# Optimization experiments

Hardware: AMD Instinct MI355X
Metric: run time of the kernel (lower is better)

## Reference

```python
import jax, jax.numpy as jnp
import numpy as np

HIDDEN = 1024
NUM_CLASSES = 10
NUM_GAUSSIANS = 8
IN_FEATURES = 16
HEADS = NUM_CLASSES * NUM_GAUSSIANS * IN_FEATURES * 2  # 2560 tiny Linear(hidden,1) heads


def setup_inputs() -> dict:
    key = jax.random.key(0)
    kx, kw, kb = jax.random.split(key, 3)
    x = jax.random.normal(kx, (8192, HIDDEN), dtype=jnp.float32)
    # Stacked weights of the 2560 per-head Linear(hidden,1) layers.
    bound = 1.0 / np.sqrt(HIDDEN)
    W = jax.random.uniform(kw, (HIDDEN, HEADS), minval=-bound, maxval=bound, dtype=jnp.float32)
    b = jax.random.uniform(kb, (HEADS,), minval=-bound, maxval=bound, dtype=jnp.float32)
    return {"x": x, "W": W, "b": b}


def reference(x, W, b):
    batch = x.shape[0]
    # Fused form of the Python loop of Linear(hidden,1)+Sigmoid per head.
    z = jax.nn.sigmoid(x @ W + b)  # [batch, HEADS]
    return z.reshape(batch, NUM_CLASSES, NUM_GAUSSIANS, IN_FEATURES, 2)
```

## Files before the change

kernel.cpp:

```cpp
#include <hip/hip_runtime.h>
#include <hip/hip_bf16.h>

#define HIDDEN 1024
#define HEADS  2560

#define BM 128
#define BN 160
#define BK 64
#define NT (HIDDEN / BK)
#define ABYT (BM * BK * 2)
#define BBYT (BN * BK * 2)
#define BUFSZ (ABYT + BBYT)

typedef float  f32x4  __attribute__((ext_vector_type(4)));
typedef __bf16 bf16x8 __attribute__((ext_vector_type(8)));
typedef __bf16 bf16x4 __attribute__((ext_vector_type(4)));

__device__ __forceinline__ void gload_lds16(const void* g, void* l) {
    __builtin_amdgcn_global_load_lds(
        (const __attribute__((address_space(1))) unsigned int*)g,
        (__attribute__((address_space(3))) unsigned int*)l, 16, 0, 0);
}
__device__ __forceinline__ unsigned swz(unsigned x) {
    return x ^ (((x >> 7) & 7u) << 4);
}

__global__ __launch_bounds__(256)
void cvt_all(const float* __restrict__ x, const float* __restrict__ W,
             __bf16* __restrict__ xc, __bf16* __restrict__ Wt, int n8)
{
    if (blockIdx.x < 640) {
        __shared__ __bf16 tile[64][72];
        const int t  = threadIdx.x;
        const int n0 = (blockIdx.x % 40) * 64;
        const int k0 = (blockIdx.x / 40) * 64;

        #pragma unroll
        for (int i = 0; i < 4; ++i) {
            const int k    = (t >> 4) + i * 16;
            const int col4 = (t & 15) * 4;
            const float4 v = *reinterpret_cast<const float4*>(
                W + (size_t)(k0 + k) * HEADS + n0 + col4);
            bf16x4 h;
            h[0] = (__bf16)v.x; h[1] = (__bf16)v.y; h[2] = (__bf16)v.z; h[3] = (__bf16)v.w;
            *reinterpret_cast<bf16x4*>(&tile[k][col4]) = h;
        }
        __syncthreads();
        #pragma unroll
        for (int i = 0; i < 4; ++i) {
            const int n  = (t >> 4) + i * 16;
            const int k4 = (t & 15) * 4;
            bf16x4 h;
            h[0] = tile[k4 + 0][n]; h[1] = tile[k4 + 1][n];
            h[2] = tile[k4 + 2][n]; h[3] = tile[k4 + 3][n];
            *reinterpret_cast<bf16x4*>(Wt + (size_t)(n0 + n) * HIDDEN + k0 + k4) = h;
        }
    } else {
        int idx    = (blockIdx.x - 640) * blockDim.x + threadIdx.x;
        int stride = (gridDim.x - 640) * blockDim.x;
        for (int i = idx; i < n8; i += stride) {
            const float4 a = *reinterpret_cast<const float4*>(x + (size_t)i * 8);
            const float4 b = *reinterpret_cast<const float4*>(x + (size_t)i * 8 + 4);
            bf16x8 h;
            h[0] = (__bf16)a.x; h[1] = (__bf16)a.y; h[2] = (__bf16)a.z; h[3] = (__bf16)a.w;
            h[4] = (__bf16)b.x; h[5] = (__bf16)b.y; h[6] = (__bf16)b.z; h[7] = (__bf16)b.w;
            *reinterpret_cast<bf16x8*>(xc + (size_t)i * 8) = h;
        }
    }
}

__global__ __launch_bounds__(512, 4)
void gemm_dl2(const __bf16* __restrict__ A, const __bf16* __restrict__ Bt,
              const float* __restrict__ bias, float* __restrict__ out)
{
    __shared__ char lds[2 * BUFSZ];

    const int t    = threadIdx.x;
    const int lane = t & 63;
    const int w    = t >> 6;
    const int wr   = w & 3;
    const int wc   = w >> 2;
    const int lhi  = lane >> 4;
    const int llo  = lane & 15;

    const int bid = blockIdx.x;
    const int by  = (bid & 7) * 2 + ((bid >> 3) & 1);
    const int bx  = bid >> 4;
    const int bm0 = bx * BM;
    const int bn0 = by * BN;

    const unsigned d0 = (unsigned)(t * 16);
    const unsigned L0 = swz(d0);
    const char* asrc0 = (const char*)A  + (size_t)(bm0 + (L0 >> 7)) * (HIDDEN * 2) + (L0 & 127);
    const char* bsrc0 = (const char*)Bt + (size_t)(bn0 + (L0 >> 7)) * (HIDDEN * 2) + (L0 & 127);
    const unsigned dt = 16384u + (unsigned)(t * 16);
    const unsigned Lt = swz(dt);
    const char* bsrct = (const char*)Bt + (size_t)(bn0 + (Lt >> 7)) * (HIDDEN * 2) + (Lt & 127);

    char* adst0 = (char*)lds + d0;
    char* bdst0 = (char*)lds + ABYT + d0;
    char* bdstt = (char*)lds + ABYT + dt;

    const unsigned xa = (unsigned)((llo & 7) << 4);
    const unsigned klo[2] = { ((unsigned)(lhi * 16)) ^ xa,
                              ((unsigned)(64 + lhi * 16)) ^ xa };
    const unsigned rowA = (unsigned)((wr * 32 + llo) * 128);
    const unsigned rowB = (unsigned)ABYT + (unsigned)((wc * 80 + llo) * 128);

    f32x4 acc[2][5];
    #pragma unroll
    for (int m = 0; m < 2; ++m)
        #pragma unroll
        for (int n = 0; n < 5; ++n)
            acc[m][n] = f32x4{0.f, 0.f, 0.f, 0.f};

    gload_lds16(asrc0,          adst0);
    gload_lds16(asrc0 + 131072, adst0 + 8192);
    gload_lds16(bsrc0,          bdst0);
    gload_lds16(bsrc0 + 131072, bdst0 + 8192);
    if (w < 4) gload_lds16(bsrct, bdstt);
    asm volatile("s_waitcnt vmcnt(0)" ::: "memory");
    __builtin_amdgcn_s_barrier();

    for (int k = 0; k < NT; ++k) {
        const char* buf  = lds + (k & 1) * BUFSZ;
        const unsigned nb = (unsigned)(((k + 1) & 1) * BUFSZ);
        const int   koff = (k + 1) * 128;

        if (k + 1 < NT) {
            gload_lds16(asrc0 + koff,          adst0 + nb);
            gload_lds16(asrc0 + koff + 131072, adst0 + nb + 8192);
            gload_lds16(bsrc0 + koff,          bdst0 + nb);
            gload_lds16(bsrc0 + koff + 131072, bdst0 + nb + 8192);
            if (w < 4) gload_lds16(bsrct + koff, bdstt + nb);
        }

        #pragma unroll
        for (int kk = 0; kk < 2; ++kk) {
            bf16x8 af[2], bfr[5];
            #pragma unroll
            for (int m = 0; m < 2; ++m)
                af[m]  = *(const bf16x8*)(buf + rowA + m * 2048 + klo[kk]);
            #pragma unroll
            for (int n = 0; n < 5; ++n)
                bfr[n] = *(const bf16x8*)(buf + rowB + n * 2048 + klo[kk]);
            #pragma unroll
            for (int m = 0; m < 2; ++m)
                #pragma unroll
                for (int n = 0; n < 5; ++n)
                    acc[m][n] = __builtin_amdgcn_mfma_f32_16x16x32_bf16(
                        af[m], bfr[n], acc[m][n], 0, 0, 0);
        }

        asm volatile("s_waitcnt vmcnt(0)" ::: "memory");
        __builtin_amdgcn_s_barrier();
    }

    #pragma unroll
    for (int n = 0; n < 5; ++n) {
        const int col  = bn0 + wc * 80 + n * 16 + llo;
        const float bv = bias[col];
        #pragma unroll
        for (int m = 0; m < 2; ++m) {
            const int row0 = bm0 + wr * 32 + m * 16 + lhi * 4;
            #pragma unroll
            for (int r = 0; r < 4; ++r) {
                const float z = acc[m][n][r] + bv;
                out[(size_t)(row0 + r) * HEADS + col] = __fdividef(1.0f, 1.0f + __expf(-z));
            }
        }
    }
}

#define FBM 128
#define FBN 128
#define FBK 32
#define FLDK 40

__global__ __launch_bounds__(256)
void lch_gemm(const float* __restrict__ x, const float* __restrict__ W,
              const float* __restrict__ b, float* __restrict__ out)
{
    __shared__ __bf16 As[FBM][FLDK];
    __shared__ __bf16 Bs[FBN][FLDK];

    const int t   = threadIdx.x;
    const int bm0 = blockIdx.x * FBM;
    const int bn0 = blockIdx.y * FBN;
    const int lane = t & 63;
    const int wid  = t >> 6;
    const int wr   = wid >> 1;
    const int wc   = wid & 1;
    const int lhi  = lane >> 4;
    const int llo  = lane & 15;

    f32x4 acc[4][4];
    #pragma unroll
    for (int i = 0; i < 4; ++i)
        #pragma unroll
        for (int j = 0; j < 4; ++j)
            acc[i][j] = f32x4{0.f, 0.f, 0.f, 0.f};

    const int bn_col  = t & 127;
    const int bk_base = (t >> 7) * 16;

    for (int k0 = 0; k0 < HIDDEN; k0 += FBK) {
        #pragma unroll
        for (int i = 0; i < 4; ++i) {
            const int f   = t + i * 256;
            const int row = f >> 3;
            const int c4  = (f & 7) * 4;
            const float4 v = *reinterpret_cast<const float4*>(
                x + (size_t)(bm0 + row) * HIDDEN + k0 + c4);
            bf16x4 h;
            h[0] = (__bf16)v.x; h[1] = (__bf16)v.y;
            h[2] = (__bf16)v.z; h[3] = (__bf16)v.w;
            *reinterpret_cast<bf16x4*>(&As[row][c4]) = h;
        }
        {
            const float* wp = W + (size_t)(k0 + bk_base) * HEADS + bn0 + bn_col;
            bf16x8 h0, h1;
            #pragma unroll
            for (int i = 0; i < 8; ++i) h0[i] = (__bf16)wp[(size_t)i * HEADS];
            #pragma unroll
            for (int i = 0; i < 8; ++i) h1[i] = (__bf16)wp[(size_t)(i + 8) * HEADS];
            *reinterpret_cast<bf16x8*>(&Bs[bn_col][bk_base])     = h0;
            *reinterpret_cast<bf16x8*>(&Bs[bn_col][bk_base + 8]) = h1;
        }
        __syncthreads();

        bf16x8 af[4], bfr[4];
        #pragma unroll
        for (int i = 0; i < 4; ++i)
            af[i] = *reinterpret_cast<const bf16x8*>(&As[wr * 64 + i * 16 + llo][lhi * 8]);
        #pragma unroll
        for (int j = 0; j < 4; ++j)
            bfr[j] = *reinterpret_cast<const bf16x8*>(&Bs[wc * 64 + j * 16 + llo][lhi * 8]);
        #pragma unroll
        for (int i = 0; i < 4; ++i)
            #pragma unroll
            for (int j = 0; j < 4; ++j)
                acc[i][j] = __builtin_amdgcn_mfma_f32_16x16x32_bf16(
                    af[i], bfr[j], acc[i][j], 0, 0, 0);
        __syncthreads();
    }

    #pragma unroll
    for (int j = 0; j < 4; ++j) {
        const int col  = bn0 + wc * 64 + j * 16 + llo;
        const float bv = b[col];
        #pragma unroll
        for (int i = 0; i < 4; ++i) {
            const int row0 = bm0 + wr * 64 + i * 16 + lhi * 4;
            #pragma unroll
            for (int r = 0; r < 4; ++r) {
                const float z = acc[i][j][r] + bv;
                out[(size_t)(row0 + r) * HEADS + col] = 1.0f / (1.0f + __expf(-z));
            }
        }
    }
}

extern "C" void kernel_launch(void* const* d_in, const int* in_sizes, int n_in,
                              void* d_out, int out_size, void* d_ws, size_t ws_size,
                              hipStream_t stream) {
    const float* x = (const float*)d_in[0];
    const float* W = (const float*)d_in[1];
    const float* b = (const float*)d_in[2];
    float* out     = (float*)d_out;

    const int M = in_sizes[0] / HIDDEN;

    const size_t xc_bytes = (size_t)M * HIDDEN * sizeof(__bf16);
    const size_t wt_bytes = (size_t)HEADS * HIDDEN * sizeof(__bf16);

    if (ws_size >= xc_bytes + wt_bytes && (M % BM) == 0) {
        __bf16* xc = (__bf16*)d_ws;
        __bf16* Wt = (__bf16*)((char*)d_ws + xc_bytes);

        cvt_all<<<640 + 2048, 256, 0, stream>>>(x, W, xc, Wt, M * HIDDEN / 8);

        const int nwg = (M / BM) * (HEADS / BN);
        gemm_dl2<<<nwg, 512, 0, stream>>>(xc, Wt, b, out);
    } else {
        dim3 grid(M / FBM, HEADS / FBN);
        lch_gemm<<<grid, dim3(256), 0, stream>>>(x, W, b, out);
    }
}
```

Before: 66.83 us.

## Fuse x fp32-to-bf16 conversion into GEMM A-tile loads

The separate pre-pass that converts x to bf16 in workspace is removed. The GEMM now loads fp32 x directly into registers, converts it, and writes the bf16 tile into swizzled LDS, with the writes issued after the MFMA loop to overlap load latency. This avoids a full write and re-read of the bf16 copy of x. In exchange, each GEMM block re-reads fp32 x, which is twice the bytes, across 16 column blocks, and adds register pressure plus a register-staged path in place of the direct global-to-LDS load.

```diff
diff --git a/kernel.cpp b/kernel.cpp
--- a/kernel.cpp
+++ b/kernel.cpp
@@ -24,54 +24,46 @@
 __device__ __forceinline__ unsigned swz(unsigned x) {
     return x ^ (((x >> 7) & 7u) << 4);
 }
+__device__ __forceinline__ bf16x8 cvt8(float4 a, float4 b) {
+    bf16x8 h;
+    h[0] = (__bf16)a.x; h[1] = (__bf16)a.y; h[2] = (__bf16)a.z; h[3] = (__bf16)a.w;
+    h[4] = (__bf16)b.x; h[5] = (__bf16)b.y; h[6] = (__bf16)b.z; h[7] = (__bf16)b.w;
+    return h;
+}
 
 __global__ __launch_bounds__(256)
-void cvt_all(const float* __restrict__ x, const float* __restrict__ W,
-             __bf16* __restrict__ xc, __bf16* __restrict__ Wt, int n8)
+void cvt_w(const float* __restrict__ W, __bf16* __restrict__ Wt)
 {
-    if (blockIdx.x < 640) {
-        __shared__ __bf16 tile[64][72];
-        const int t  = threadIdx.x;
-        const int n0 = (blockIdx.x % 40) * 64;
-        const int k0 = (blockIdx.x / 40) * 64;
-
-        #pragma unroll
-        for (int i = 0; i < 4; ++i) {
-            const int k    = (t >> 4) + i * 16;
-            const int col4 = (t & 15) * 4;
-            const float4 v = *reinterpret_cast<const float4*>(
-                W + (size_t)(k0 + k) * HEADS + n0 + col4);
-            bf16x4 h;
-            h[0] = (__bf16)v.x; h[1] = (__bf16)v.y; h[2] = (__bf16)v.z; h[3] = (__bf16)v.w;
-            *reinterpret_cast<bf16x4*>(&tile[k][col4]) = h;
-        }
-        __syncthreads();
-        #pragma unroll
-        for (int i = 0; i < 4; ++i) {
-            const int n  = (t >> 4) + i * 16;
-            const int k4 = (t & 15) * 4;
-            bf16x4 h;
-            h[0] = tile[k4 + 0][n]; h[1] = tile[k4 + 1][n];
-            h[2] = tile[k4 + 2][n]; h[3] = tile[k4 + 3][n];
-            *reinterpret_cast<bf16x4*>(Wt + (size_t)(n0 + n) * HIDDEN + k0 + k4) = h;
-        }
-    } else {
-        int idx    = (blockIdx.x - 640) * blockDim.x + threadIdx.x;
-        int stride = (gridDim.x - 640) * blockDim.x;
-        for (int i = idx; i < n8; i += stride) {
-            const float4 a = *reinterpret_cast<const float4*>(x + (size_t)i * 8);
-            const float4 b = *reinterpret_cast<const float4*>(x + (size_t)i * 8 + 4);
-            bf16x8 h;
-            h[0] = (__bf16)a.x; h[1] = (__bf16)a.y; h[2] = (__bf16)a.z; h[3] = (__bf16)a.w;
-            h[4] = (__bf16)b.x; h[5] = (__bf16)b.y; h[6] = (__bf16)b.z; h[7] = (__bf16)b.w;
-            *reinterpret_cast<bf16x8*>(xc + (size_t)i * 8) = h;
-        }
+    __shared__ __bf16 tile[64][72];
+    const int t  = threadIdx.x;
+    const int n0 = (blockIdx.x % 40) * 64;
+    const int k0 = (blockIdx.x / 40) * 64;
+
+    #pragma unroll
+    for (int i = 0; i < 4; ++i) {
+        const int k    = (t >> 4) + i * 16;
+        const int col4 = (t & 15) * 4;
+        const float4 v = *reinterpret_cast<const float4*>(
+            W + (size_t)(k0 + k) * HEADS + n0 + col4);
+        bf16x4 h;
+        h[0] = (__bf16)v.x; h[1] = (__bf16)v.y; h[2] = (__bf16)v.z; h[3] = (__bf16)v.w;
+        *reinterpret_cast<bf16x4*>(&tile[k][col4]) = h;
+    }
+    __syncthreads();
+    #pragma unroll
+    for (int i = 0; i < 4; ++i) {
+        const int n  = (t >> 4) + i * 16;
+        const int k4 = (t & 15) * 4;
+        bf16x4 h;
+        h[0] = tile[k4 + 0][n]; h[1] = tile[k4 + 1][n];
+        h[2] = tile[k4 + 2][n]; h[3] = tile[k4 + 3][n];
+        *reinterpret_cast<bf16x4*>(Wt + (size_t)(n0 + n) * HIDDEN + k0 + k4) = h;
     }
 }
 
 __global__ __launch_bounds__(512, 4)
-void gemm_dl2(const __bf16* __restrict__ A, const __bf16* __restrict__ Bt,
-              const float* __restrict__ bias, float* __restrict__ out)
+void gemm_fx(const float* __restrict__ x, const __bf16* __restrict__ Bt,
+             const float* __restrict__ bias, float* __restrict__ out)
 {
     __shared__ char lds[2 * BUFSZ];
 
@@ -91,11 +83,14 @@
 
     const unsigned d0 = (unsigned)(t * 16);
     const unsigned L0 = swz(d0);
-    const char* asrc0 = (const char*)A  + (size_t)(bm0 + (L0 >> 7)) * (HIDDEN * 2) + (L0 & 127);
-    const char* bsrc0 = (const char*)Bt + (size_t)(bn0 + (L0 >> 7)) * (HIDDEN * 2) + (L0 & 127);
+    const char* xsrc0 = (const char*)x
+        + (size_t)(bm0 + (L0 >> 7)) * 4096 + ((L0 & 127) << 1);
+    const char* bsrc0 = (const char*)Bt
+        + (size_t)(bn0 + (L0 >> 7)) * 2048 + (L0 & 127);
     const unsigned dt = 16384u + (unsigned)(t * 16);
     const unsigned Lt = swz(dt);
-    const char* bsrct = (const char*)Bt + (size_t)(bn0 + (Lt >> 7)) * (HIDDEN * 2) + (Lt & 127);
+    const char* bsrct = (const char*)Bt
+        + (size_t)(bn0 + (Lt >> 7)) * 2048 + (Lt & 127);
 
     char* adst0 = (char*)lds + d0;
     char* bdst0 = (char*)lds + ABYT + d0;
@@ -114,25 +109,36 @@
         for (int n = 0; n < 5; ++n)
             acc[m][n] = f32x4{0.f, 0.f, 0.f, 0.f};
 
-    gload_lds16(asrc0,          adst0);
-    gload_lds16(asrc0 + 131072, adst0 + 8192);
-    gload_lds16(bsrc0,          bdst0);
-    gload_lds16(bsrc0 + 131072, bdst0 + 8192);
-    if (w < 4) gload_lds16(bsrct, bdstt);
-    asm volatile("s_waitcnt vmcnt(0)" ::: "memory");
+    {
+        float4 fa0 = *reinterpret_cast<const float4*>(xsrc0);
+        float4 fb0 = *reinterpret_cast<const float4*>(xsrc0 + 16);
+        float4 fa1 = *reinterpret_cast<const float4*>(xsrc0 + 262144);
+        float4 fb1 = *reinterpret_cast<const float4*>(xsrc0 + 262144 + 16);
+        gload_lds16(bsrc0,          bdst0);
+        gload_lds16(bsrc0 + 131072, bdst0 + 8192);
+        if (w < 4) gload_lds16(bsrct, bdstt);
+        *reinterpret_cast<bf16x8*>(adst0)        = cvt8(fa0, fb0);
+        *reinterpret_cast<bf16x8*>(adst0 + 8192) = cvt8(fa1, fb1);
+    }
+    asm volatile("s_waitcnt vmcnt(0) lgkmcnt(0)" ::: "memory");
     __builtin_amdgcn_s_barrier();
 
     for (int k = 0; k < NT; ++k) {
         const char* buf  = lds + (k & 1) * BUFSZ;
         const unsigned nb = (unsigned)(((k + 1) & 1) * BUFSZ);
-        const int   koff = (k + 1) * 128;
-
-        if (k + 1 < NT) {
-            gload_lds16(asrc0 + koff,          adst0 + nb);
-            gload_lds16(asrc0 + koff + 131072, adst0 + nb + 8192);
-            gload_lds16(bsrc0 + koff,          bdst0 + nb);
-            gload_lds16(bsrc0 + koff + 131072, bdst0 + nb + 8192);
-            if (w < 4) gload_lds16(bsrct + koff, bdstt + nb);
+        const int   kb = (k + 1) * 128;
+        const int   kf = (k + 1) * 256;
+        const bool  st = (k + 1 < NT);
+
+        float4 fa0, fb0, fa1, fb1;
+        if (st) {
+            fa0 = *reinterpret_cast<const float4*>(xsrc0 + kf);
+            fb0 = *reinterpret_cast<const float4*>(xsrc0 + kf + 16);
+            fa1 = *reinterpret_cast<const float4*>(xsrc0 + kf + 262144);
+            fb1 = *reinterpret_cast<const float4*>(xsrc0 + kf + 262144 + 16);
+            gload_lds16(bsrc0 + kb,          bdst0 + nb);
+            gload_lds16(bsrc0 + kb + 131072, bdst0 + nb + 8192);
+            if (w < 4) gload_lds16(bsrct + kb, bdstt + nb);
         }
 
         #pragma unroll
@@ -152,7 +158,12 @@
                         af[m], bfr[n], acc[m][n], 0, 0, 0);
         }
 
-        asm volatile("s_waitcnt vmcnt(0)" ::: "memory");
+        if (st) {
+            *reinterpret_cast<bf16x8*>(adst0 + nb)        = cvt8(fa0, fb0);
+            *reinterpret_cast<bf16x8*>(adst0 + nb + 8192) = cvt8(fa1, fb1);
+        }
+
+        asm volatile("s_waitcnt vmcnt(0) lgkmcnt(0)" ::: "memory");
         __builtin_amdgcn_s_barrier();
     }
 
@@ -271,17 +282,15 @@
 
     const int M = in_sizes[0] / HIDDEN;
 
-    const size_t xc_bytes = (size_t)M * HIDDEN * sizeof(__bf16);
     const size_t wt_bytes = (size_t)HEADS * HIDDEN * sizeof(__bf16);
 
-    if (ws_size >= xc_bytes + wt_bytes && (M % BM) == 0) {
-        __bf16* xc = (__bf16*)d_ws;
-        __bf16* Wt = (__bf16*)((char*)d_ws + xc_bytes);
-
-        cvt_all<<<640 + 2048, 256, 0, stream>>>(x, W, xc, Wt, M * HIDDEN / 8);
+    if (ws_size >= wt_bytes && (M % BM) == 0) {
+        __bf16* Wt = (__bf16*)d_ws;
+
+        cvt_w<<<dim3(40 * (HIDDEN / 64)), 256, 0, stream>>>(W, Wt);
 
         const int nwg = (M / BM) * (HEADS / BN);
-        gemm_dl2<<<nwg, 512, 0, stream>>>(xc, Wt, b, out);
+        gemm_fx<<<nwg, 512, 0, stream>>>(x, Wt, b, out);
     } else {
         dim3 grid(M / FBM, HEADS / FBN);
         lch_gemm<<<grid, dim3(256), 0, stream>>>(x, W, b, out);
```

Measured after the change: 77.18 us. 1.16x slower.
